# Performance work log

Measured on AMD Instinct MI355X. Metric: run time of the kernel, lower is better.

## Reference

```python
import jax, jax.numpy as jnp
import numpy as np

EMB_DIM = 1024
NUM_HEADS = 16
SCALE_WEIGHTS = 1.0
TINY = jnp.finfo(jnp.float32).tiny


def setup_inputs() -> dict:
    key = jax.random.key(0)
    k1, k2, k3 = jax.random.split(key, 3)
    B, S = 2, 2048
    x = jax.random.normal(k1, (B, S, EMB_DIM), dtype=jnp.float32)
    weights = jax.random.uniform(k2, (B, S), dtype=jnp.float32)
    W_qkv = jax.random.normal(k3, (EMB_DIM, 3 * EMB_DIM), dtype=jnp.float32) / np.sqrt(EMB_DIM)
    b_qkv = jnp.zeros((3 * EMB_DIM,), dtype=jnp.float32)
    return {"x": x, "weights": weights, "W_qkv": W_qkv, "b_qkv": b_qkv}


def reference(x, weights, W_qkv, b_qkv):
    B, S, E = x.shape
    H = NUM_HEADS
    hd = E // H
    # QKV projection: [B,S,3E] -> [B,H,S,3*hd] -> split
    qkv = x @ W_qkv + b_qkv
    qkv = qkv.reshape(B, S, H, 3 * hd).transpose(0, 2, 1, 3)
    q, k, v = jnp.split(qkv, 3, axis=-1)  # each [B,H,S,hd]
    # weights: [B,S] -> [B,1,1,S] (broadcast over heads and query positions)
    w = weights[:, None, None, :]
    # scores with log-weight bias and hard masks
    attn_logits = jnp.einsum("bhqd,bhkd->bhqk", q, k) / jnp.sqrt(jnp.asarray(hd, x.dtype))
    attn_logits = attn_logits + jnp.log(w / SCALE_WEIGHTS + TINY)
    attn_logits = jnp.where(w == 0, -9e15, attn_logits)
    attn_logits = jnp.where(w == 1, 9e15, attn_logits)
    attention = jax.nn.softmax(attn_logits, axis=-1)
    values = jnp.einsum("bhqk,bhkd->bhqd", attention, v)
    return values.transpose(0, 2, 1, 3).reshape(B, S, E)
```

## Files before the change

kernel.cpp:

```cpp
#include <hip/hip_runtime.h>
#include <math.h>

#define B_  2
#define S_  2048
#define E_  1024
#define H_  16
#define HD_ 64
#define N3_ 3072
#define M_  (B_*S_)

typedef _Float16 h8  __attribute__((ext_vector_type(8)));
typedef _Float16 h4  __attribute__((ext_vector_type(4)));
typedef _Float16 h2  __attribute__((ext_vector_type(2)));
typedef __fp16   fp16x2 __attribute__((ext_vector_type(2)));
typedef float    f4  __attribute__((ext_vector_type(4)));
typedef float    fv16 __attribute__((ext_vector_type(16)));

typedef __attribute__((address_space(3))) unsigned int       lds_u32;
typedef const __attribute__((address_space(1))) unsigned int glob_u32;

__device__ __forceinline__ void gld16(const void* g, void* l) {
    __builtin_amdgcn_global_load_lds((glob_u32*)g, (lds_u32*)l, 16, 0, 0);
}
__device__ __forceinline__ float exp2_hw(float x) { return __builtin_amdgcn_exp2f(x); }
__device__ __forceinline__ float fmax3(float a, float b, float c) {
    return fmaxf(fmaxf(a, b), c);
}
__device__ __forceinline__ h2 cvt_pk_f16(float a, float b) {
    fp16x2 r = __builtin_amdgcn_cvt_pkrtz(a, b);
    return __builtin_bit_cast(h2, r);
}

#define QSCALE 0.18033688011112042f
#define RESCALE_THR 8.0f

__global__ __launch_bounds__(256) void prep_kernel(
        const float* __restrict__ x, _Float16* __restrict__ x16,
        const float* __restrict__ w, _Float16* __restrict__ w16,
        const float* __restrict__ W, _Float16* __restrict__ Wt) {
    __shared__ float T[64][65];
    int L = blockIdx.x;
    int tid = threadIdx.x;
    if (L < 2050) {
        const float* src = (L < 2048) ? &x[(size_t)L * 2048] : &w[(size_t)(L - 2048) * 2048];
        _Float16* dst    = (L < 2048) ? &x16[(size_t)L * 2048] : &w16[(size_t)(L - 2048) * 2048];
        int i = tid * 8;
        float4 u = *(const float4*)&src[i];
        float4 v = *(const float4*)&src[i + 4];
        h8 o;
        o[0] = (_Float16)u.x; o[1] = (_Float16)u.y; o[2] = (_Float16)u.z; o[3] = (_Float16)u.w;
        o[4] = (_Float16)v.x; o[5] = (_Float16)v.y; o[6] = (_Float16)v.z; o[7] = (_Float16)v.w;
        *(h8*)&dst[i] = o;
    } else {
        int L2 = L - 2050;
        int k0 = (L2 & 15) * 64, n0 = (L2 >> 4) * 64;
        int r = tid >> 4, c4 = (tid & 15) * 4;
#pragma unroll
        for (int i = 0; i < 4; i++) {
            int row = r + i * 16;
            float4 u = *(const float4*)&W[(size_t)(k0 + row) * N3_ + n0 + c4];
            T[c4 + 0][row] = u.x; T[c4 + 1][row] = u.y;
            T[c4 + 2][row] = u.z; T[c4 + 3][row] = u.w;
        }
        __syncthreads();
#pragma unroll
        for (int i = 0; i < 4; i++) {
            int rn = r + i * 16;
            h4 p;
            p[0] = (_Float16)T[rn][c4 + 0]; p[1] = (_Float16)T[rn][c4 + 1];
            p[2] = (_Float16)T[rn][c4 + 2]; p[3] = (_Float16)T[rn][c4 + 3];
            *(h4*)&Wt[(size_t)(n0 + rn) * E_ + k0 + c4] = p;
        }
    }
}

__global__ __launch_bounds__(256, 2) void qkv_gemm32(
        const _Float16* __restrict__ x16, const _Float16* __restrict__ wt,
        const float* __restrict__ bq, const float* __restrict__ w,
        _Float16* __restrict__ qws, _Float16* __restrict__ kws,
        _Float16* __restrict__ vtws) {
    __shared__ __align__(16) _Float16 Ab[2][128 * 64];
    __shared__ __align__(16) _Float16 Wb[2][192 * 64];

    int tid = threadIdx.x;
    int wid = tid >> 6, lane = tid & 63;
    int l31 = lane & 31, hi = lane >> 5, l7 = l31 & 7;
    int srow = lane >> 3;
    int wm = wid & 1, wn = wid >> 1;

    int L = blockIdx.x;
    int head = 2 * (L & 7) + (L >> 8);
    int mb = (L >> 3) & 31;
    int m0 = mb * 128;
    int n0 = head * 192;
    int b = m0 >> 11;
    int bh = b * H_ + head;
    int sblk = m0 & 2047;

    fv16 acc[2][3];
#pragma unroll
    for (int ntl = 0; ntl < 3; ntl++) {
        int n_abs = wn * 96 + ntl * 32;
        int which = n_abs >> 6;
        fv16 ini;
        if (which == 2) {
            float bb = bq[n0 + n_abs + l31];
#pragma unroll
            for (int r = 0; r < 16; r++) ini[r] = bb;
        } else {
#pragma unroll
            for (int g = 0; g < 4; g++) {
                f4 bv = *(const f4*)&bq[n0 + n_abs + 8 * g + 4 * hi];
#pragma unroll
                for (int j = 0; j < 4; j++) ini[4 * g + j] = bv[j];
            }
        }
        acc[0][ntl] = ini; acc[1][ntl] = ini;
    }

    auto stage = [&](int t, int bf) {
        int k0 = t * 64;
#pragma unroll
        for (int j = 0; j < 4; j++) {
            int batch = wid * 4 + j;
            int row = batch * 8 + srow;
            int ch = (lane & 7) ^ srow ^ (batch & 7);
            gld16(&x16[(size_t)(m0 + row) * E_ + k0 + ch * 8], &Ab[bf][batch * 8 * 64]);
        }
#pragma unroll
        for (int j = 0; j < 6; j++) {
            int batch = wid * 6 + j;
            int row = batch * 8 + srow;
            int ch = (lane & 7) ^ srow ^ (batch & 7);
            gld16(&wt[(size_t)(n0 + row) * E_ + k0 + ch * 8], &Wb[bf][batch * 8 * 64]);
        }
    };

    stage(0, 0);

    for (int t = 0; t < 16; t++) {
        int bf = t & 1;
        __syncthreads();
        if (t < 15) stage(t + 1, bf ^ 1);
#pragma unroll
        for (int step = 0; step < 4; step++) {
            h8 af[2], wf[3];
#pragma unroll
            for (int mt = 0; mt < 2; mt++) {
                int R = wm * 64 + mt * 32 + l31;
                int ph = ((2 * step + hi) ^ l7 ^ ((mt * 4 + (l31 >> 3)) & 7)) * 8;
                af[mt] = *(const h8*)&Ab[bf][R * 64 + ph];
            }
#pragma unroll
            for (int ntl = 0; ntl < 3; ntl++) {
                int R = wn * 96 + ntl * 32 + l31;
                int ph = ((2 * step + hi) ^ l7 ^ ((wn * 12 + ntl * 4 + (l31 >> 3)) & 7)) * 8;
                wf[ntl] = *(const h8*)&Wb[bf][R * 64 + ph];
            }
#pragma unroll
            for (int ntl = 0; ntl < 3; ntl++) {
                bool isv = (wn == 1) && (ntl >= 1);
#pragma unroll
                for (int mt = 0; mt < 2; mt++) {
                    if (isv)
                        acc[mt][ntl] = __builtin_amdgcn_mfma_f32_32x32x16_f16(af[mt], wf[ntl], acc[mt][ntl], 0, 0, 0);
                    else
                        acc[mt][ntl] = __builtin_amdgcn_mfma_f32_32x32x16_f16(wf[ntl], af[mt], acc[mt][ntl], 0, 0, 0);
                }
            }
        }
    }

#pragma unroll
    for (int ntl = 0; ntl < 3; ntl++) {
        int n_abs = wn * 96 + ntl * 32;
        int which = n_abs >> 6;
#pragma unroll
        for (int mt = 0; mt < 2; mt++) {
            if (which == 2) {
                int d = (n_abs & 63) + l31;
#pragma unroll
                for (int g = 0; g < 4; g++) {
                    int soff = wm * 64 + mt * 32 + 8 * g + 4 * hi;
                    f4 wf4 = *(const f4*)&w[m0 + soff];
                    h4 p;
#pragma unroll
                    for (int j = 0; j < 4; j++)
                        p[j] = (_Float16)(acc[mt][ntl][4 * g + j] * wf4[j]);
                    *(h4*)&vtws[((size_t)bh * 64 + d) * S_ + sblk + soff] = p;
                }
            } else {
                _Float16* dst = (which == 0) ? qws : kws;
                float scale = (which == 0) ? QSCALE : 1.0f;
                int s = sblk + wm * 64 + mt * 32 + l31;
#pragma unroll
                for (int g = 0; g < 4; g++) {
                    int d0 = (n_abs & 63) + 8 * g + 4 * hi;
                    h4 p;
#pragma unroll
                    for (int j = 0; j < 4; j++)
                        p[j] = (_Float16)(acc[mt][ntl][4 * g + j] * scale);
                    *(h4*)&dst[((size_t)bh * S_ + s) * 64 + d0] = p;
                }
            }
        }
    }
}

__global__ __launch_bounds__(256, 2) void attn_kernel(
        const _Float16* __restrict__ q, const _Float16* __restrict__ k,
        const _Float16* __restrict__ vt, const _Float16* __restrict__ w16,
        float* __restrict__ out) {
    __shared__ __align__(16) _Float16 Kb[2][64 * 64];
    __shared__ __align__(16) _Float16 Vb[2][64 * 64];
    __shared__ __align__(16) _Float16 lws16[2048];

    int tid = threadIdx.x;
    int wid = tid >> 6, lane = tid & 63;
    int l31 = lane & 31, hi = lane >> 5, l7 = l31 & 7;
    int srow = lane >> 3;
    int L = blockIdx.x;
    int bh = (L & 7) + 8 * (L >> 7);
    int qt = (L >> 3) & 15;
    int q0 = qt * 128;
    int b = bh >> 4, h = bh & 15;

    const _Float16* qbase = q + (size_t)bh * S_ * HD_;
    const _Float16* kbase = k + (size_t)bh * S_ * HD_;
    const _Float16* vbase = vt + (size_t)bh * HD_ * S_;
    const _Float16* wbase = w16 + (size_t)b * S_;

    gld16(&wbase[wid * 512 + lane * 8], &lws16[wid * 512]);

    auto stage = [&](int kt, int bf) {
        int k0 = kt * 64;
#pragma unroll
        for (int j = 0; j < 2; j++) {
            int batch = wid * 2 + j;
            int row = batch * 8 + srow;
            int ch = (lane & 7) ^ srow ^ (batch & 7);
            gld16(&kbase[(size_t)(k0 + row) * 64 + ch * 8], &Kb[bf][batch * 8 * 64]);
            gld16(&vbase[(size_t)row * S_ + k0 + ch * 8], &Vb[bf][batch * 8 * 64]);
        }
    };

    stage(0, 0);

    int qrow = q0 + wid * 32 + l31;
    h8 qf[4];
#pragma unroll
    for (int step = 0; step < 4; step++)
        qf[step] = *(const h8*)&qbase[(size_t)qrow * 64 + 16 * step + 8 * hi];

    fv16 o[2], ol;
    o[0] = (fv16)0.0f; o[1] = (fv16)0.0f; ol = (fv16)0.0f;
    float m_r = -INFINITY;

    for (int kt = 0; kt < 32; kt++) {
        int bf = kt & 1;
        __syncthreads();
        if (kt < 31) stage(kt + 1, bf ^ 1);

        fv16 st[2];
        st[0] = (fv16)0.0f; st[1] = (fv16)0.0f;
        __builtin_amdgcn_s_setprio(1);
#pragma unroll
        for (int step = 0; step < 4; step++) {
#pragma unroll
            for (int kt2 = 0; kt2 < 2; kt2++) {
                int R = kt2 * 32 + l31;
                int ph = ((2 * step + hi) ^ l7 ^ ((kt2 * 4 + (l31 >> 3)) & 7)) * 8;
                h8 kf = *(const h8*)&Kb[bf][R * 64 + ph];
                st[kt2] = __builtin_amdgcn_mfma_f32_32x32x16_f16(kf, qf[step], st[kt2], 0, 0, 0);
            }
        }
        __builtin_amdgcn_s_setprio(0);

        float tm[11];
#pragma unroll
        for (int r = 0; r < 10; r++)
            tm[r] = fmax3(st[(3*r)>>4][(3*r)&15], st[(3*r+1)>>4][(3*r+1)&15],
                          st[(3*r+2)>>4][(3*r+2)&15]);
        tm[10] = fmaxf(st[1][14], st[1][15]);
        float u0 = fmax3(tm[0], tm[1], tm[2]);
        float u1 = fmax3(tm[3], tm[4], tm[5]);
        float u2 = fmax3(tm[6], tm[7], tm[8]);
        float u3 = fmaxf(tm[9], tm[10]);
        float pmax = fmaxf(fmax3(u0, u1, u2), u3);

        if (!__all(pmax <= m_r + RESCALE_THR)) {
            float rowmax = fmaxf(pmax, __shfl_xor(pmax, 32));
            float mnew = fmaxf(m_r, rowmax);
            float alpha = exp2_hw(m_r - mnew);
            m_r = mnew;
            o[0] = o[0] * alpha;
            o[1] = o[1] * alpha;
            ol = ol * alpha;
        }

        h4 pf[2][4];
#pragma unroll
        for (int kt2 = 0; kt2 < 2; kt2++)
#pragma unroll
            for (int g = 0; g < 4; g++) {
                float e0 = exp2_hw(st[kt2][4 * g + 0] - m_r);
                float e1 = exp2_hw(st[kt2][4 * g + 1] - m_r);
                float e2 = exp2_hw(st[kt2][4 * g + 2] - m_r);
                float e3 = exp2_hw(st[kt2][4 * g + 3] - m_r);
                h2 p01 = cvt_pk_f16(e0, e1);
                h2 p23 = cvt_pk_f16(e2, e3);
                h4 p;
                p[0] = p01[0]; p[1] = p01[1]; p[2] = p23[0]; p[3] = p23[1];
                pf[kt2][g] = p;
            }

        int k0 = kt * 64;
        __builtin_amdgcn_s_setprio(1);
#pragma unroll
        for (int kt2 = 0; kt2 < 2; kt2++)
#pragma unroll
            for (int g = 0; g < 4; g++) {
                int c = 4 * kt2 + g;
#pragma unroll
                for (int dt = 0; dt < 2; dt++) {
                    int R = dt * 32 + l31;
                    int ph = (c ^ l7 ^ ((dt * 4 + (l31 >> 3)) & 7)) * 8 + hi * 4;
                    h4 vf = *(const h4*)&Vb[bf][R * 64 + ph];
                    o[dt] = __builtin_amdgcn_mfma_f32_32x32x8f16(vf, pf[kt2][g], o[dt], 0, 0, 0);
                }
                h4 wf_ = *(const h4*)&lws16[k0 + c * 8 + 4 * hi];
                ol = __builtin_amdgcn_mfma_f32_32x32x8f16(wf_, pf[kt2][g], ol, 0, 0, 0);
            }
        __builtin_amdgcn_s_setprio(0);
    }

    float linv = 1.0f / ol[0];
    float* obase = &out[((size_t)(b * S_ + qrow)) * E_ + h * 64];
#pragma unroll
    for (int dt = 0; dt < 2; dt++)
#pragma unroll
        for (int g = 0; g < 4; g++) {
            int d0 = dt * 32 + 8 * g + 4 * hi;
            f4 ov;
#pragma unroll
            for (int j = 0; j < 4; j++) ov[j] = o[dt][4 * g + j] * linv;
            *(f4*)&obase[d0] = ov;
        }
}

extern "C" void kernel_launch(void* const* d_in, const int* in_sizes, int n_in,
                              void* d_out, int out_size, void* d_ws, size_t ws_size,
                              hipStream_t stream) {
    const float* x  = (const float*)d_in[0];
    const float* w  = (const float*)d_in[1];
    const float* Wq = (const float*)d_in[2];
    const float* bq = (const float*)d_in[3];
    float* out = (float*)d_out;

    char* p = (char*)d_ws;
    _Float16* x16 = (_Float16*)p;              p += (size_t)M_ * E_ * 2;
    _Float16* wt  = (_Float16*)p;              p += (size_t)E_ * N3_ * 2;
    _Float16* qb  = (_Float16*)p;              p += (size_t)M_ * E_ * 2;
    _Float16* kb  = (_Float16*)p;              p += (size_t)M_ * E_ * 2;
    _Float16* vtb = (_Float16*)p;              p += (size_t)M_ * HD_ * H_ * 2;
    _Float16* w16 = (_Float16*)p;

    prep_kernel<<<dim3(2050 + 768), dim3(256), 0, stream>>>(x, x16, w, w16, Wq, wt);
    qkv_gemm32<<<dim3(512), dim3(256), 0, stream>>>(x16, wt, bq, w, qb, kb, vtb);
    attn_kernel<<<dim3(512), dim3(256), 0, stream>>>(qb, kb, vtb, w16, out);
}
```

Before: 178.9 us.

## Split PV accumulators, prefetch V fragments early, and remap QKV GEMM block order

Result: slower. 185.5 us (+3.7%).

```diff
diff --git a/kernel.cpp b/kernel.cpp
--- a/kernel.cpp
+++ b/kernel.cpp
@@ -89,8 +89,9 @@
     int wm = wid & 1, wn = wid >> 1;
 
     int L = blockIdx.x;
-    int head = 2 * (L & 7) + (L >> 8);
-    int mb = (L >> 3) & 31;
+    int tL = L >> 3;
+    int head = tL & 15;
+    int mb = (L & 7) * 4 + (tL >> 4);
     int m0 = mb * 128;
     int n0 = head * 192;
     int b = m0 >> 11;
@@ -252,8 +253,10 @@
     for (int step = 0; step < 4; step++)
         qf[step] = *(const h8*)&qbase[(size_t)qrow * 64 + 16 * step + 8 * hi];
 
-    fv16 o[2], ol;
-    o[0] = (fv16)0.0f; o[1] = (fv16)0.0f; ol = (fv16)0.0f;
+    fv16 oa[2], ob[2], ola, olb;
+    oa[0] = (fv16)0.0f; oa[1] = (fv16)0.0f;
+    ob[0] = (fv16)0.0f; ob[1] = (fv16)0.0f;
+    ola = (fv16)0.0f; olb = (fv16)0.0f;
     float m_r = -INFINITY;
 
     for (int kt = 0; kt < 32; kt++) {
@@ -275,6 +278,19 @@
             }
         }
         __builtin_amdgcn_s_setprio(0);
+
+        int k0 = kt * 64;
+        h4 vf[2][8], wfv[8];
+#pragma unroll
+        for (int c = 0; c < 8; c++) {
+#pragma unroll
+            for (int dt = 0; dt < 2; dt++) {
+                int R = dt * 32 + l31;
+                int ph = (c ^ l7 ^ ((dt * 4 + (l31 >> 3)) & 7)) * 8 + hi * 4;
+                vf[dt][c] = *(const h4*)&Vb[bf][R * 64 + ph];
+            }
+            wfv[c] = *(const h4*)&lws16[k0 + c * 8 + 4 * hi];
+        }
 
         float tm[11];
 #pragma unroll
@@ -293,12 +309,12 @@
             float mnew = fmaxf(m_r, rowmax);
             float alpha = exp2_hw(m_r - mnew);
             m_r = mnew;
-            o[0] = o[0] * alpha;
-            o[1] = o[1] * alpha;
-            ol = ol * alpha;
-        }
-
-        h4 pf[2][4];
+            oa[0] = oa[0] * alpha; oa[1] = oa[1] * alpha;
+            ob[0] = ob[0] * alpha; ob[1] = ob[1] * alpha;
+            ola = ola * alpha; olb = olb * alpha;
+        }
+
+        h4 pf[8];
 #pragma unroll
         for (int kt2 = 0; kt2 < 2; kt2++)
 #pragma unroll
@@ -311,30 +327,29 @@
                 h2 p23 = cvt_pk_f16(e2, e3);
                 h4 p;
                 p[0] = p01[0]; p[1] = p01[1]; p[2] = p23[0]; p[3] = p23[1];
-                pf[kt2][g] = p;
-            }
-
-        int k0 = kt * 64;
+                pf[kt2 * 4 + g] = p;
+            }
+
         __builtin_amdgcn_s_setprio(1);
 #pragma unroll
-        for (int kt2 = 0; kt2 < 2; kt2++)
-#pragma unroll
-            for (int g = 0; g < 4; g++) {
-                int c = 4 * kt2 + g;
-#pragma unroll
-                for (int dt = 0; dt < 2; dt++) {
-                    int R = dt * 32 + l31;
-                    int ph = (c ^ l7 ^ ((dt * 4 + (l31 >> 3)) & 7)) * 8 + hi * 4;
-                    h4 vf = *(const h4*)&Vb[bf][R * 64 + ph];
-                    o[dt] = __builtin_amdgcn_mfma_f32_32x32x8f16(vf, pf[kt2][g], o[dt], 0, 0, 0);
-                }
-                h4 wf_ = *(const h4*)&lws16[k0 + c * 8 + 4 * hi];
-                ol = __builtin_amdgcn_mfma_f32_32x32x8f16(wf_, pf[kt2][g], ol, 0, 0, 0);
-            }
+        for (int c = 0; c < 8; c++) {
+            if (c & 1) {
+#pragma unroll
+                for (int dt = 0; dt < 2; dt++)
+                    ob[dt] = __builtin_amdgcn_mfma_f32_32x32x8f16(vf[dt][c], pf[c], ob[dt], 0, 0, 0);
+                olb = __builtin_amdgcn_mfma_f32_32x32x8f16(wfv[c], pf[c], olb, 0, 0, 0);
+            } else {
+#pragma unroll
+                for (int dt = 0; dt < 2; dt++)
+                    oa[dt] = __builtin_amdgcn_mfma_f32_32x32x8f16(vf[dt][c], pf[c], oa[dt], 0, 0, 0);
+                ola = __builtin_amdgcn_mfma_f32_32x32x8f16(wfv[c], pf[c], ola, 0, 0, 0);
+            }
+        }
         __builtin_amdgcn_s_setprio(0);
     }
 
-    float linv = 1.0f / ol[0];
+    float lsum = ola[0] + olb[0];
+    float linv = 1.0f / lsum;
     float* obase = &out[((size_t)(b * S_ + qrow)) * E_ + h * 64];
 #pragma unroll
     for (int dt = 0; dt < 2; dt++)
@@ -343,7 +358,8 @@
             int d0 = dt * 32 + 8 * g + 4 * hi;
             f4 ov;
 #pragma unroll
-            for (int j = 0; j < 4; j++) ov[j] = o[dt][4 * g + j] * linv;
+            for (int j = 0; j < 4; j++)
+                ov[j] = (oa[dt][4 * g + j] + ob[dt][4 * g + j]) * linv;
             *(f4*)&obase[d0] = ov;
         }
 }
```

## Software-pipeline attention loop: overlap next QK^T and softmax with current PV

Applied to the files above, without the earlier changes.

Result: no change. 178.2 us (-0.4%).

```diff
diff --git a/kernel.cpp b/kernel.cpp
--- a/kernel.cpp
+++ b/kernel.cpp
@@ -212,7 +212,7 @@
         const _Float16* __restrict__ vt, const _Float16* __restrict__ w16,
         float* __restrict__ out) {
     __shared__ __align__(16) _Float16 Kb[2][64 * 64];
-    __shared__ __align__(16) _Float16 Vb[2][64 * 64];
+    __shared__ __align__(16) _Float16 Vb[3][64 * 64];
     __shared__ __align__(16) _Float16 lws16[2048];
 
     int tid = threadIdx.x;
@@ -232,19 +232,21 @@
 
     gld16(&wbase[wid * 512 + lane * 8], &lws16[wid * 512]);
 
-    auto stage = [&](int kt, int bf) {
+    auto vptr = [&](int i) -> _Float16* {
+        return (i == 0) ? &Vb[0][0] : ((i == 1) ? &Vb[1][0] : &Vb[2][0]);
+    };
+
+    auto stage_kv = [&](int kt, _Float16* kdst, _Float16* vdst) {
         int k0 = kt * 64;
 #pragma unroll
         for (int j = 0; j < 2; j++) {
             int batch = wid * 2 + j;
             int row = batch * 8 + srow;
-            int ch = (lane & 7) ^ srow ^ (batch & 7);
-            gld16(&kbase[(size_t)(k0 + row) * 64 + ch * 8], &Kb[bf][batch * 8 * 64]);
-            gld16(&vbase[(size_t)row * S_ + k0 + ch * 8], &Vb[bf][batch * 8 * 64]);
-        }
-    };
-
-    stage(0, 0);
+            int ch = l7 ^ srow ^ (batch & 7);
+            gld16(&kbase[(size_t)(k0 + row) * 64 + ch * 8], &kdst[batch * 8 * 64]);
+            gld16(&vbase[(size_t)row * S_ + k0 + ch * 8], &vdst[batch * 8 * 64]);
+        }
+    };
 
     int qrow = q0 + wid * 32 + l31;
     h8 qf[4];
@@ -256,32 +258,28 @@
     o[0] = (fv16)0.0f; o[1] = (fv16)0.0f; ol = (fv16)0.0f;
     float m_r = -INFINITY;
 
-    for (int kt = 0; kt < 32; kt++) {
-        int bf = kt & 1;
-        __syncthreads();
-        if (kt < 31) stage(kt + 1, bf ^ 1);
-
-        fv16 st[2];
-        st[0] = (fv16)0.0f; st[1] = (fv16)0.0f;
+    auto qkt = [&](const _Float16* kbuf, fv16* stl) {
+        stl[0] = (fv16)0.0f; stl[1] = (fv16)0.0f;
         __builtin_amdgcn_s_setprio(1);
 #pragma unroll
-        for (int step = 0; step < 4; step++) {
+        for (int step = 0; step < 4; step++)
 #pragma unroll
             for (int kt2 = 0; kt2 < 2; kt2++) {
                 int R = kt2 * 32 + l31;
                 int ph = ((2 * step + hi) ^ l7 ^ ((kt2 * 4 + (l31 >> 3)) & 7)) * 8;
-                h8 kf = *(const h8*)&Kb[bf][R * 64 + ph];
-                st[kt2] = __builtin_amdgcn_mfma_f32_32x32x16_f16(kf, qf[step], st[kt2], 0, 0, 0);
-            }
-        }
+                h8 kf = *(const h8*)&kbuf[R * 64 + ph];
+                stl[kt2] = __builtin_amdgcn_mfma_f32_32x32x16_f16(kf, qf[step], stl[kt2], 0, 0, 0);
+            }
         __builtin_amdgcn_s_setprio(0);
-
+    };
+
+    auto softmax = [&](const fv16* stl, h4* pf) {
         float tm[11];
 #pragma unroll
         for (int r = 0; r < 10; r++)
-            tm[r] = fmax3(st[(3*r)>>4][(3*r)&15], st[(3*r+1)>>4][(3*r+1)&15],
-                          st[(3*r+2)>>4][(3*r+2)&15]);
-        tm[10] = fmaxf(st[1][14], st[1][15]);
+            tm[r] = fmax3(stl[(3*r)>>4][(3*r)&15], stl[(3*r+1)>>4][(3*r+1)&15],
+                          stl[(3*r+2)>>4][(3*r+2)&15]);
+        tm[10] = fmaxf(stl[1][14], stl[1][15]);
         float u0 = fmax3(tm[0], tm[1], tm[2]);
         float u1 = fmax3(tm[3], tm[4], tm[5]);
         float u2 = fmax3(tm[6], tm[7], tm[8]);
@@ -298,23 +296,23 @@
             ol = ol * alpha;
         }
 
-        h4 pf[2][4];
 #pragma unroll
         for (int kt2 = 0; kt2 < 2; kt2++)
 #pragma unroll
             for (int g = 0; g < 4; g++) {
-                float e0 = exp2_hw(st[kt2][4 * g + 0] - m_r);
-                float e1 = exp2_hw(st[kt2][4 * g + 1] - m_r);
-                float e2 = exp2_hw(st[kt2][4 * g + 2] - m_r);
-                float e3 = exp2_hw(st[kt2][4 * g + 3] - m_r);
+                float e0 = exp2_hw(stl[kt2][4 * g + 0] - m_r);
+                float e1 = exp2_hw(stl[kt2][4 * g + 1] - m_r);
+                float e2 = exp2_hw(stl[kt2][4 * g + 2] - m_r);
+                float e3 = exp2_hw(stl[kt2][4 * g + 3] - m_r);
                 h2 p01 = cvt_pk_f16(e0, e1);
                 h2 p23 = cvt_pk_f16(e2, e3);
                 h4 p;
                 p[0] = p01[0]; p[1] = p01[1]; p[2] = p23[0]; p[3] = p23[1];
-                pf[kt2][g] = p;
-            }
-
-        int k0 = kt * 64;
+                pf[kt2 * 4 + g] = p;
+            }
+    };
+
+    auto pv = [&](const _Float16* vbuf, const h4* pf, int k0w) {
         __builtin_amdgcn_s_setprio(1);
 #pragma unroll
         for (int kt2 = 0; kt2 < 2; kt2++)
@@ -325,13 +323,46 @@
                 for (int dt = 0; dt < 2; dt++) {
                     int R = dt * 32 + l31;
                     int ph = (c ^ l7 ^ ((dt * 4 + (l31 >> 3)) & 7)) * 8 + hi * 4;
-                    h4 vf = *(const h4*)&Vb[bf][R * 64 + ph];
-                    o[dt] = __builtin_amdgcn_mfma_f32_32x32x8f16(vf, pf[kt2][g], o[dt], 0, 0, 0);
+                    h4 vf = *(const h4*)&vbuf[R * 64 + ph];
+                    o[dt] = __builtin_amdgcn_mfma_f32_32x32x8f16(vf, pf[c], o[dt], 0, 0, 0);
                 }
-                h4 wf_ = *(const h4*)&lws16[k0 + c * 8 + 4 * hi];
-                ol = __builtin_amdgcn_mfma_f32_32x32x8f16(wf_, pf[kt2][g], ol, 0, 0, 0);
+                h4 wf_ = *(const h4*)&lws16[k0w + c * 8 + 4 * hi];
+                ol = __builtin_amdgcn_mfma_f32_32x32x8f16(wf_, pf[c], ol, 0, 0, 0);
             }
         __builtin_amdgcn_s_setprio(0);
+    };
+
+    stage_kv(0, &Kb[0][0], &Vb[0][0]);
+    __syncthreads();
+    stage_kv(1, &Kb[1][0], &Vb[1][0]);
+
+    fv16 st[2];
+    h4 pfA[8], pfB[8];
+    qkt(&Kb[0][0], st);
+    softmax(st, pfA);
+
+    int vc = 0;
+    for (int t = 0; t < 16; t++) {
+        {
+            int kt = 2 * t;
+            __syncthreads();
+            int vs = vc + 2; if (vs >= 3) vs -= 3;
+            if (kt < 30) stage_kv(kt + 2, &Kb[0][0], vptr(vs));
+            if (kt < 31) qkt(&Kb[1][0], st);
+            pv(vptr(vc), pfA, kt * 64);
+            if (kt < 31) softmax(st, pfB);
+            vc = (vc == 2) ? 0 : vc + 1;
+        }
+        {
+            int kt = 2 * t + 1;
+            __syncthreads();
+            int vs = vc + 2; if (vs >= 3) vs -= 3;
+            if (kt < 30) stage_kv(kt + 2, &Kb[1][0], vptr(vs));
+            if (kt < 31) qkt(&Kb[0][0], st);
+            pv(vptr(vc), pfB, kt * 64);
+            if (kt < 31) softmax(st, pfA);
+            vc = (vc == 2) ? 0 : vc + 1;
+        }
     }
 
     float linv = 1.0f / ol[0];
```
